# Kernel tuning notes

Hardware: AMD Instinct MI355X
Metric: run time of the kernel (lower is better)

## Reference

```python
import jax, jax.numpy as jnp
import numpy as np

N = 100000
E = 1600000
IN_DIM = 256
HID = 256
OUT = 64
K = 10
ALPHA = 0.1


def setup_inputs() -> dict:
    key = jax.random.key(0)
    ks = jax.random.split(key, 8)
    x = jax.random.normal(ks[0], (N, IN_DIM), dtype=jnp.float32)
    edge_index = jax.random.randint(ks[1], (2, E), 0, N, dtype=jnp.int64)
    # Linear params (torch default-ish scale)
    W1 = jax.random.normal(ks[2], (IN_DIM, HID), dtype=jnp.float32) / np.sqrt(IN_DIM)
    b1 = jnp.zeros((HID,), dtype=jnp.float32)
    W2 = jax.random.normal(ks[3], (HID, OUT), dtype=jnp.float32) / np.sqrt(HID)
    b2 = jnp.zeros((OUT,), dtype=jnp.float32)
    alpha = jnp.asarray([ALPHA * (1.0 - ALPHA) ** k for k in range(K + 1)], dtype=jnp.float32)
    return {"x": x, "edge_index": edge_index, "W1": W1, "b1": b1, "W2": W2, "b2": b2, "alpha": alpha}


def reference(x, edge_index, W1, b1, W2, b2, alpha):
    # MLP head (dropout = identity in eval)
    h = jax.nn.relu(x @ W1 + b1) @ W2 + b2  # [N, OUT]

    row, col = edge_index[0], edge_index[1]
    num_nodes = h.shape[0]
    # degree over row (matches torch_geometric degree(row, ...))
    deg = jax.ops.segment_sum(jnp.ones_like(row, dtype=h.dtype), row, num_segments=num_nodes)
    deg_inv_sqrt = jnp.where(deg > 0, jax.lax.rsqrt(jnp.maximum(deg, 1.0)), 0.0)
    norm = deg_inv_sqrt[row] * deg_inv_sqrt[col]  # [E]

    gamma = jax.nn.softmax(alpha)

    def step(carry, g):
        h_cur, acc = carry
        msg = h_cur[col] * norm[:, None]  # gather + scale  [E, OUT]
        h_new = jax.ops.segment_sum(msg, row, num_segments=num_nodes)  # scatter_add
        return (h_new, acc + g * h_new), None

    acc0 = gamma[0] * h
    (_, out), _ = jax.lax.scan(step, (h, acc0), gamma[1:])
    return out
```

## Files before the change

kernel.cpp:

```cpp
#include <hip/hip_runtime.h>
#include <hip/hip_bf16.h>

#define N_NODES 100000
#define N_EDGES 1600000
#define IN_DIM_ 256
#define HID_ 256
#define OUT_ 64
#define KSTEPS 10

typedef __attribute__((ext_vector_type(4))) float f32x4;
typedef __attribute__((ext_vector_type(8))) __bf16 bf16x8;
typedef __attribute__((ext_vector_type(8))) unsigned short u16x8;

static __device__ __forceinline__ unsigned short f2bf(float f) {
    union { float f; unsigned int u; } v; v.f = f;
    unsigned int u = v.u;
    unsigned int r = u + 0x7FFFu + ((u >> 16) & 1u);
    return (unsigned short)(r >> 16);
}
static __device__ __forceinline__ float bflo(unsigned int v) {
    return __uint_as_float(v << 16);
}
static __device__ __forceinline__ float bfhi(unsigned int v) {
    return __uint_as_float(v & 0xFFFF0000u);
}


__global__ void gamma_kernel(const float* __restrict__ alpha, float* __restrict__ gamma) {
    if (threadIdx.x == 0) {
        float m = alpha[0];
        for (int i = 1; i <= KSTEPS; ++i) m = fmaxf(m, alpha[i]);
        float e[KSTEPS + 1];
        float s = 0.f;
        for (int i = 0; i <= KSTEPS; ++i) { e[i] = expf(alpha[i] - m); s += e[i]; }
        float inv = 1.f / s;
        for (int i = 0; i <= KSTEPS; ++i) gamma[i] = e[i] * inv;
    }
}

__global__ void deg_kernel(const int* __restrict__ row, int* __restrict__ deg, int E) {
    int e = blockIdx.x * 256 + threadIdx.x;
    if (e < E) atomicAdd(&deg[row[e]], 1);
}

__global__ void dis_kernel(const int* __restrict__ deg, float* __restrict__ dis, int n) {
    int i = blockIdx.x * 256 + threadIdx.x;
    if (i < n) {
        int d = deg[i];
        dis[i] = d > 0 ? rsqrtf((float)d) : 0.f;
    }
}


__global__ __launch_bounds__(256) void scan_sum_kernel(const int* __restrict__ deg,
                                                       int* __restrict__ bsum, int n) {
    __shared__ int s[256];
    int t = threadIdx.x;
    int i = blockIdx.x * 256 + t;
    s[t] = (i < n) ? deg[i] : 0;
    __syncthreads();
    for (int st = 128; st > 0; st >>= 1) {
        if (t < st) s[t] += s[t + st];
        __syncthreads();
    }
    if (t == 0) bsum[blockIdx.x] = s[0];
}

__global__ __launch_bounds__(512) void scan_block_kernel(int* __restrict__ bsum,
                                                         int* __restrict__ off,
                                                         int nblk, int n) {
    __shared__ int s[512];
    int t = threadIdx.x;
    int v = (t < nblk) ? bsum[t] : 0;
    s[t] = v;
    __syncthreads();
    for (int st = 1; st < 512; st <<= 1) {
        int a = (t >= st) ? s[t - st] : 0;
        __syncthreads();
        s[t] += a;
        __syncthreads();
    }
    if (t < nblk) bsum[t] = s[t] - v;
    if (t == 511) off[n] = s[511];
}

__global__ __launch_bounds__(256) void scan_final_kernel(const int* __restrict__ deg,
                                                         const int* __restrict__ bsum,
                                                         int* __restrict__ off, int n) {
    __shared__ int s[256];
    int t = threadIdx.x;
    int i = blockIdx.x * 256 + t;
    int v = (i < n) ? deg[i] : 0;
    s[t] = v;
    __syncthreads();
    for (int st = 1; st < 256; st <<= 1) {
        int a = (t >= st) ? s[t - st] : 0;
        __syncthreads();
        s[t] += a;
        __syncthreads();
    }
    if (i < n) off[i] = bsum[blockIdx.x] + s[t] - v;
}

__global__ void csr_scatter_kernel(const int* __restrict__ row, const int* __restrict__ col,
                                   const float* __restrict__ dis, const int* __restrict__ off,
                                   int* __restrict__ cursor, int2* __restrict__ ecsr, int E) {
    int e = blockIdx.x * 256 + threadIdx.x;
    if (e < E) {
        int r = row[e], c = col[e];
        float w = dis[r] * dis[c];
        int pos = atomicAdd(&cursor[r], 1);
        int2 p;
        p.x = c;
        p.y = __float_as_int(w);
        ecsr[(size_t)off[r] + pos] = p;
    }
}


__global__ __launch_bounds__(256) void gemm1_kernel(const float* __restrict__ x,
                                                    const float* __restrict__ W1,
                                                    const float* __restrict__ b1,
                                                    unsigned short* __restrict__ h1, int M) {
    __shared__ unsigned short As[64][40];
    __shared__ unsigned short Bs[64][40];

    const int tid = threadIdx.x;
    const int lane = tid & 63;
    const int w = tid >> 6;
    const int wr = w >> 1, wc = w & 1;
    const int row0 = blockIdx.x * 64;
    const int n0 = blockIdx.y * 64;

    const int am = tid >> 2;
    const int ak = (tid & 3) * 8;
    const int bk = tid >> 3;
    const int bn = (tid & 7) * 8;

    f32x4 acc[2][2] = {};

    for (int kk = 0; kk < 256; kk += 32) {
        {
            int gr = row0 + am;
            u16x8 av;
            if (gr < M) {
                const float* p = x + (size_t)gr * IN_DIM_ + kk + ak;
                #pragma unroll
                for (int j = 0; j < 8; ++j) av[j] = f2bf(p[j]);
            } else {
                #pragma unroll
                for (int j = 0; j < 8; ++j) av[j] = 0;
            }
            *(u16x8*)&As[am][ak] = av;
        }
        {
            const float* p = W1 + (size_t)(kk + bk) * HID_ + n0 + bn;
            #pragma unroll
            for (int j = 0; j < 8; ++j) Bs[bn + j][bk] = f2bf(p[j]);
        }
        __syncthreads();

        const int fr = lane & 15;
        const int ko = (lane >> 4) * 8;
        bf16x8 a[2], b[2];
        #pragma unroll
        for (int mi = 0; mi < 2; ++mi) a[mi] = *(const bf16x8*)&As[wr * 32 + mi * 16 + fr][ko];
        #pragma unroll
        for (int ni = 0; ni < 2; ++ni) b[ni] = *(const bf16x8*)&Bs[wc * 32 + ni * 16 + fr][ko];
        #pragma unroll
        for (int mi = 0; mi < 2; ++mi)
            #pragma unroll
            for (int ni = 0; ni < 2; ++ni)
                acc[mi][ni] = __builtin_amdgcn_mfma_f32_16x16x32_bf16(a[mi], b[ni], acc[mi][ni], 0, 0, 0);
        __syncthreads();
    }

    const int fr = lane & 15;
    const int rg = (lane >> 4) * 4;
    #pragma unroll
    for (int mi = 0; mi < 2; ++mi) {
        #pragma unroll
        for (int r = 0; r < 4; ++r) {
            int gm = row0 + wr * 32 + mi * 16 + rg + r;
            if (gm < M) {
                #pragma unroll
                for (int ni = 0; ni < 2; ++ni) {
                    int gn = n0 + wc * 32 + ni * 16 + fr;
                    float v = acc[mi][ni][r] + b1[gn];
                    v = fmaxf(v, 0.f);
                    h1[(size_t)gm * HID_ + gn] = f2bf(v);
                }
            }
        }
    }
}

__global__ __launch_bounds__(256) void gemm2_kernel(const unsigned short* __restrict__ h1,
                                                    const float* __restrict__ W2,
                                                    const float* __restrict__ b2,
                                                    const float* __restrict__ gamma,
                                                    unsigned short* __restrict__ h,
                                                    float* __restrict__ out, int M) {
    __shared__ unsigned short As[64][40];
    __shared__ unsigned short Bs[64][40];

    const int tid = threadIdx.x;
    const int lane = tid & 63;
    const int w = tid >> 6;
    const int wr = w >> 1, wc = w & 1;
    const int row0 = blockIdx.x * 64;

    const int am = tid >> 2;
    const int ak = (tid & 3) * 8;
    const int bk = tid >> 3;
    const int bn = (tid & 7) * 8;

    f32x4 acc[2][2] = {};

    for (int kk = 0; kk < 256; kk += 32) {
        {
            int gr = row0 + am;
            if (gr < M) {
                *(u16x8*)&As[am][ak] = *(const u16x8*)&h1[(size_t)gr * HID_ + kk + ak];
            } else {
                u16x8 z = {};
                *(u16x8*)&As[am][ak] = z;
            }
        }
        {
            const float* p = W2 + (size_t)(kk + bk) * OUT_ + bn;
            #pragma unroll
            for (int j = 0; j < 8; ++j) Bs[bn + j][bk] = f2bf(p[j]);
        }
        __syncthreads();

        const int fr = lane & 15;
        const int ko = (lane >> 4) * 8;
        bf16x8 a[2], b[2];
        #pragma unroll
        for (int mi = 0; mi < 2; ++mi) a[mi] = *(const bf16x8*)&As[wr * 32 + mi * 16 + fr][ko];
        #pragma unroll
        for (int ni = 0; ni < 2; ++ni) b[ni] = *(const bf16x8*)&Bs[wc * 32 + ni * 16 + fr][ko];
        #pragma unroll
        for (int mi = 0; mi < 2; ++mi)
            #pragma unroll
            for (int ni = 0; ni < 2; ++ni)
                acc[mi][ni] = __builtin_amdgcn_mfma_f32_16x16x32_bf16(a[mi], b[ni], acc[mi][ni], 0, 0, 0);
        __syncthreads();
    }

    const float g0 = gamma[0];
    const int fr = lane & 15;
    const int rg = (lane >> 4) * 4;
    #pragma unroll
    for (int mi = 0; mi < 2; ++mi) {
        #pragma unroll
        for (int r = 0; r < 4; ++r) {
            int gm = row0 + wr * 32 + mi * 16 + rg + r;
            if (gm < M) {
                #pragma unroll
                for (int ni = 0; ni < 2; ++ni) {
                    int gn = wc * 32 + ni * 16 + fr;
                    float v = acc[mi][ni][r] + b2[gn];
                    h[(size_t)gm * OUT_ + gn] = f2bf(v);
                    out[(size_t)gm * OUT_ + gn] = g0 * v;
                }
            }
        }
    }
}

__global__ __launch_bounds__(256) void pull_kernel(const int* __restrict__ off,
                                                   const int2* __restrict__ ecsr,
                                                   const unsigned short* __restrict__ hc,
                                                   unsigned short* __restrict__ hn,
                                                   float* __restrict__ out,
                                                   const float* __restrict__ gamma,
                                                   int k, int n) {
    int node = blockIdx.x * 4 + (threadIdx.x >> 6);
    if (node >= n) return;
    int lane = threadIdx.x & 63;
    int half = lane >> 5;
    int fl = (lane & 31) * 2;
    int s = off[node], e = off[node + 1];
    float acc0 = 0.f, acc1 = 0.f;

    int j = s + half;
    for (; j + 2 < e; j += 4) {
        int2 pa = ecsr[j];
        int2 pb = ecsr[j + 2];
        unsigned int va = *(const unsigned int*)&hc[(size_t)pa.x * OUT_ + fl];
        unsigned int vb = *(const unsigned int*)&hc[(size_t)pb.x * OUT_ + fl];
        float wa = __int_as_float(pa.y);
        float wb = __int_as_float(pb.y);
        acc0 += wa * bflo(va);
        acc1 += wa * bfhi(va);
        acc0 += wb * bflo(vb);
        acc1 += wb * bfhi(vb);
    }
    if (j < e) {
        int2 p = ecsr[j];
        unsigned int v = *(const unsigned int*)&hc[(size_t)p.x * OUT_ + fl];
        float w = __int_as_float(p.y);
        acc0 += w * bflo(v);
        acc1 += w * bfhi(v);
    }

    acc0 += __shfl_xor(acc0, 32);
    acc1 += __shfl_xor(acc1, 32);

    if (lane < 32) {
        float g = gamma[k];
        size_t o = (size_t)node * OUT_ + fl;
        unsigned int packed = (unsigned int)f2bf(acc0) | ((unsigned int)f2bf(acc1) << 16);
        *(unsigned int*)&hn[o] = packed;
        float2* op = (float2*)&out[o];
        float2 ov = *op;
        ov.x += g * acc0;
        ov.y += g * acc1;
        *op = ov;
    }
}

extern "C" void kernel_launch(void* const* d_in, const int* in_sizes, int n_in,
                              void* d_out, int out_size, void* d_ws, size_t ws_size,
                              hipStream_t stream) {
    const float* x = (const float*)d_in[0];
    const int* ei = (const int*)d_in[1];
    const float* W1 = (const float*)d_in[2];
    const float* b1 = (const float*)d_in[3];
    const float* W2 = (const float*)d_in[4];
    const float* b2 = (const float*)d_in[5];
    const float* alpha = (const float*)d_in[6];
    const int* row = ei;
    const int* col = ei + N_EDGES;
    float* out = (float*)d_out;

    const int NBLK = (N_NODES + 255) / 256;

    char* wsb = (char*)d_ws;
    size_t p = 0;
    auto alloc = [&](size_t bytes) { size_t r = p; p += (bytes + 255) & ~255ull; return r; };
    float* gamma = (float*)(wsb + alloc(16 * 4));
    int* off     = (int*)(wsb + alloc((N_NODES + 1) * 4));
    int* cursor  = (int*)(wsb + alloc(N_NODES * 4));
    int* deg     = (int*)(wsb + alloc(N_NODES * 4));
    float* dis   = (float*)(wsb + alloc(N_NODES * 4));
    int* bsum    = (int*)(wsb + alloc(512 * 4));
    int2* ecsr   = (int2*)(wsb + alloc((size_t)N_EDGES * 8));
    unsigned short* h1  = (unsigned short*)(wsb + alloc((size_t)N_NODES * HID_ * 2));
    unsigned short* h_a = (unsigned short*)(wsb + alloc((size_t)N_NODES * OUT_ * 2));
    unsigned short* h_b = h1;

    hipMemsetAsync(cursor, 0, N_NODES * sizeof(int), stream);
    hipMemsetAsync(deg, 0, N_NODES * sizeof(int), stream);
    gamma_kernel<<<1, 64, 0, stream>>>(alpha, gamma);
    deg_kernel<<<(N_EDGES + 255) / 256, 256, 0, stream>>>(row, deg, N_EDGES);
    dis_kernel<<<NBLK, 256, 0, stream>>>(deg, dis, N_NODES);
    scan_sum_kernel<<<NBLK, 256, 0, stream>>>(deg, bsum, N_NODES);
    scan_block_kernel<<<1, 512, 0, stream>>>(bsum, off, NBLK, N_NODES);
    scan_final_kernel<<<NBLK, 256, 0, stream>>>(deg, bsum, off, N_NODES);
    csr_scatter_kernel<<<(N_EDGES + 255) / 256, 256, 0, stream>>>(row, col, dis, off, cursor,
                                                                  ecsr, N_EDGES);

    gemm1_kernel<<<dim3((N_NODES + 63) / 64, HID_ / 64), 256, 0, stream>>>(x, W1, b1, h1, N_NODES);
    gemm2_kernel<<<dim3((N_NODES + 63) / 64, 1), 256, 0, stream>>>(h1, W2, b2, gamma, h_a, out,
                                                                   N_NODES);

    unsigned short* hc = h_a;
    unsigned short* hn = h_b;
    for (int k = 1; k <= KSTEPS; ++k) {
        pull_kernel<<<(N_NODES + 3) / 4, 256, 0, stream>>>(off, ecsr, hc, hn, out, gamma, k,
                                                           N_NODES);
        unsigned short* t = hc; hc = hn; hn = t;
    }
}
```

Measured before the change: 893.3 us.

## Pre-transpose weights to bf16 and widen gemm1 tile to full hidden width

Adds a small kernel that converts W1 and W2 to transposed bf16 once, so the GEMM kernels load B tiles with vector copies instead of converting strided fp32 per block. gemm1 now computes all 256 hidden columns per block, which reads and converts each x row from fp32 once instead of four times. The pull kernel loop is unrolled to 8 edges to keep more gathers in flight. The wider gemm1 tile uses more accumulator registers and LDS, which may lower occupancy.

```diff
diff --git a/kernel.cpp b/kernel.cpp
--- a/kernel.cpp
+++ b/kernel.cpp
@@ -49,6 +49,13 @@
         int d = deg[i];
         dis[i] = d > 0 ? rsqrtf((float)d) : 0.f;
     }
+}
+
+__global__ void wcast_kernel(const float* __restrict__ W, unsigned short* __restrict__ wT,
+                             int K, int N) {
+    int k = blockIdx.x * 256 + threadIdx.x;
+    int n = blockIdx.y;
+    if (k < K) wT[(size_t)n * K + k] = f2bf(W[(size_t)k * N + n]);
 }
 
 
@@ -117,27 +124,23 @@
     }
 }
 
-
 __global__ __launch_bounds__(256) void gemm1_kernel(const float* __restrict__ x,
-                                                    const float* __restrict__ W1,
+                                                    const unsigned short* __restrict__ w1T,
                                                     const float* __restrict__ b1,
                                                     unsigned short* __restrict__ h1, int M) {
     __shared__ unsigned short As[64][40];
-    __shared__ unsigned short Bs[64][40];
+    __shared__ unsigned short Bs[256][40];
 
     const int tid = threadIdx.x;
     const int lane = tid & 63;
     const int w = tid >> 6;
     const int wr = w >> 1, wc = w & 1;
     const int row0 = blockIdx.x * 64;
-    const int n0 = blockIdx.y * 64;
 
     const int am = tid >> 2;
     const int ak = (tid & 3) * 8;
-    const int bk = tid >> 3;
-    const int bn = (tid & 7) * 8;
-
-    f32x4 acc[2][2] = {};
+
+    f32x4 acc[2][8] = {};
 
     for (int kk = 0; kk < 256; kk += 32) {
         {
@@ -154,24 +157,26 @@
             *(u16x8*)&As[am][ak] = av;
         }
         {
-            const float* p = W1 + (size_t)(kk + bk) * HID_ + n0 + bn;
-            #pragma unroll
-            for (int j = 0; j < 8; ++j) Bs[bn + j][bk] = f2bf(p[j]);
+            const unsigned short* p = w1T + (size_t)tid * 256 + kk;
+            *(u16x8*)&Bs[tid][0]  = *(const u16x8*)&p[0];
+            *(u16x8*)&Bs[tid][8]  = *(const u16x8*)&p[8];
+            *(u16x8*)&Bs[tid][16] = *(const u16x8*)&p[16];
+            *(u16x8*)&Bs[tid][24] = *(const u16x8*)&p[24];
         }
         __syncthreads();
 
         const int fr = lane & 15;
         const int ko = (lane >> 4) * 8;
-        bf16x8 a[2], b[2];
+        bf16x8 a[2];
         #pragma unroll
         for (int mi = 0; mi < 2; ++mi) a[mi] = *(const bf16x8*)&As[wr * 32 + mi * 16 + fr][ko];
         #pragma unroll
-        for (int ni = 0; ni < 2; ++ni) b[ni] = *(const bf16x8*)&Bs[wc * 32 + ni * 16 + fr][ko];
-        #pragma unroll
-        for (int mi = 0; mi < 2; ++mi)
+        for (int ni = 0; ni < 8; ++ni) {
+            bf16x8 b = *(const bf16x8*)&Bs[wc * 128 + ni * 16 + fr][ko];
             #pragma unroll
-            for (int ni = 0; ni < 2; ++ni)
-                acc[mi][ni] = __builtin_amdgcn_mfma_f32_16x16x32_bf16(a[mi], b[ni], acc[mi][ni], 0, 0, 0);
+            for (int mi = 0; mi < 2; ++mi)
+                acc[mi][ni] = __builtin_amdgcn_mfma_f32_16x16x32_bf16(a[mi], b, acc[mi][ni], 0, 0, 0);
+        }
         __syncthreads();
     }
 
@@ -184,8 +189,8 @@
             int gm = row0 + wr * 32 + mi * 16 + rg + r;
             if (gm < M) {
                 #pragma unroll
-                for (int ni = 0; ni < 2; ++ni) {
-                    int gn = n0 + wc * 32 + ni * 16 + fr;
+                for (int ni = 0; ni < 8; ++ni) {
+                    int gn = wc * 128 + ni * 16 + fr;
                     float v = acc[mi][ni][r] + b1[gn];
                     v = fmaxf(v, 0.f);
                     h1[(size_t)gm * HID_ + gn] = f2bf(v);
@@ -196,7 +201,7 @@
 }
 
 __global__ __launch_bounds__(256) void gemm2_kernel(const unsigned short* __restrict__ h1,
-                                                    const float* __restrict__ W2,
+                                                    const unsigned short* __restrict__ w2T,
                                                     const float* __restrict__ b2,
                                                     const float* __restrict__ gamma,
                                                     unsigned short* __restrict__ h,
@@ -212,8 +217,6 @@
 
     const int am = tid >> 2;
     const int ak = (tid & 3) * 8;
-    const int bk = tid >> 3;
-    const int bn = (tid & 7) * 8;
 
     f32x4 acc[2][2] = {};
 
@@ -227,10 +230,11 @@
                 *(u16x8*)&As[am][ak] = z;
             }
         }
-        {
-            const float* p = W2 + (size_t)(kk + bk) * OUT_ + bn;
-            #pragma unroll
-            for (int j = 0; j < 8; ++j) Bs[bn + j][bk] = f2bf(p[j]);
+        if (tid < 128) {
+            int n = tid >> 1, hf = (tid & 1) * 16;
+            const unsigned short* p = &w2T[(size_t)n * 256 + kk + hf];
+            *(u16x8*)&Bs[n][hf]     = *(const u16x8*)&p[0];
+            *(u16x8*)&Bs[n][hf + 8] = *(const u16x8*)&p[8];
         }
         __syncthreads();
 
@@ -286,17 +290,30 @@
     float acc0 = 0.f, acc1 = 0.f;
 
     int j = s + half;
+    for (; j + 6 < e; j += 8) {
+        int2 pa = ecsr[j];
+        int2 pb = ecsr[j + 2];
+        int2 pc = ecsr[j + 4];
+        int2 pd = ecsr[j + 6];
+        unsigned int va = *(const unsigned int*)&hc[(size_t)pa.x * OUT_ + fl];
+        unsigned int vb = *(const unsigned int*)&hc[(size_t)pb.x * OUT_ + fl];
+        unsigned int vc = *(const unsigned int*)&hc[(size_t)pc.x * OUT_ + fl];
+        unsigned int vd = *(const unsigned int*)&hc[(size_t)pd.x * OUT_ + fl];
+        float wa = __int_as_float(pa.y), wb = __int_as_float(pb.y);
+        float wc = __int_as_float(pc.y), wd = __int_as_float(pd.y);
+        acc0 += wa * bflo(va); acc1 += wa * bfhi(va);
+        acc0 += wb * bflo(vb); acc1 += wb * bfhi(vb);
+        acc0 += wc * bflo(vc); acc1 += wc * bfhi(vc);
+        acc0 += wd * bflo(vd); acc1 += wd * bfhi(vd);
+    }
     for (; j + 2 < e; j += 4) {
         int2 pa = ecsr[j];
         int2 pb = ecsr[j + 2];
         unsigned int va = *(const unsigned int*)&hc[(size_t)pa.x * OUT_ + fl];
         unsigned int vb = *(const unsigned int*)&hc[(size_t)pb.x * OUT_ + fl];
-        float wa = __int_as_float(pa.y);
-        float wb = __int_as_float(pb.y);
-        acc0 += wa * bflo(va);
-        acc1 += wa * bfhi(va);
-        acc0 += wb * bflo(vb);
-        acc1 += wb * bfhi(vb);
+        float wa = __int_as_float(pa.y), wb = __int_as_float(pb.y);
+        acc0 += wa * bflo(va); acc1 += wa * bfhi(va);
+        acc0 += wb * bflo(vb); acc1 += wb * bfhi(vb);
     }
     if (j < e) {
         int2 p = ecsr[j];
@@ -347,6 +364,8 @@
     int* deg     = (int*)(wsb + alloc(N_NODES * 4));
     float* dis   = (float*)(wsb + alloc(N_NODES * 4));
     int* bsum    = (int*)(wsb + alloc(512 * 4));
+    unsigned short* w1T = (unsigned short*)(wsb + alloc((size_t)IN_DIM_ * HID_ * 2));
+    unsigned short* w2T = (unsigned short*)(wsb + alloc((size_t)HID_ * OUT_ * 2));
     int2* ecsr   = (int2*)(wsb + alloc((size_t)N_EDGES * 8));
     unsigned short* h1  = (unsigned short*)(wsb + alloc((size_t)N_NODES * HID_ * 2));
     unsigned short* h_a = (unsigned short*)(wsb + alloc((size_t)N_NODES * OUT_ * 2));
@@ -362,10 +381,11 @@
     scan_final_kernel<<<NBLK, 256, 0, stream>>>(deg, bsum, off, N_NODES);
     csr_scatter_kernel<<<(N_EDGES + 255) / 256, 256, 0, stream>>>(row, col, dis, off, cursor,
                                                                   ecsr, N_EDGES);
-
-    gemm1_kernel<<<dim3((N_NODES + 63) / 64, HID_ / 64), 256, 0, stream>>>(x, W1, b1, h1, N_NODES);
-    gemm2_kernel<<<dim3((N_NODES + 63) / 64, 1), 256, 0, stream>>>(h1, W2, b2, gamma, h_a, out,
-                                                                   N_NODES);
+    wcast_kernel<<<dim3(1, HID_), 256, 0, stream>>>(W1, w1T, IN_DIM_, HID_);
+    wcast_kernel<<<dim3(1, OUT_), 256, 0, stream>>>(W2, w2T, HID_, OUT_);
+
+    gemm1_kernel<<<(N_NODES + 63) / 64, 256, 0, stream>>>(x, w1T, b1, h1, N_NODES);
+    gemm2_kernel<<<(N_NODES + 63) / 64, 256, 0, stream>>>(h1, w2T, b2, gamma, h_a, out, N_NODES);
 
     unsigned short* hc = h_a;
     unsigned short* hn = h_b;
```

After: 790.0 us. 11.6% less time.
